# Optimization experiments

Hardware: AMD Instinct MI355X
Metric: run time of the kernel (lower is better)

The kernel has to match this reference:

```python
import jax, jax.numpy as jnp
import numpy as np

H, D = 8, 16
HD = H * D
SCALE0 = float(1.0 / np.sqrt(D * 1))   # degree-0 dot-product scale (order m=1)
SCALE1 = float(1.0 / np.sqrt(D * 3))   # degree-1 dot-product scale (order m=3)
SHARED = float(np.sqrt(0.5))           # shared_scale = sqrt(1/2) for DOT_PROD + SHARED
NEG = -1e9


def _split_heads_q(x):  # (b,n,HD,m) -> (b,H,n,D,m)
    b, n, _, m = x.shape
    return x.reshape(b, n, H, D, m).transpose(0, 2, 1, 3, 4)


def _split_heads_k(x):  # (b,n,N,HD,m) -> (b,H,n,N,D,m)
    b, n, N, _, m = x.shape
    return x.reshape(b, n, N, H, D, m).transpose(0, 3, 1, 2, 4, 5)


def _augment_kv(k, v, feats, W_self, null_k, null_v):
    # attend_self: VNLinear self key/value; use_null_kv: learned null tokens.
    b, n = feats.shape[:2]
    m = feats.shape[-1]
    skv = jnp.einsum('oc,bncm->bnom', W_self, feats)          # (b,n,2HD,m)
    sk, sv = jnp.split(skv, 2, axis=-2)
    sk = _split_heads_q(sk)[:, :, :, None]                     # (b,H,n,1,D,m)
    sv = _split_heads_q(sv)[:, :, :, None]
    nk = jnp.broadcast_to(null_k[None, :, None, None], (b, H, n, 1, D, m))
    nv = jnp.broadcast_to(null_v[None, :, None, None], (b, H, n, 1, D, m))
    k = jnp.concatenate([nk, sk, k], axis=3)                   # (b,H,n,2+N,D,m)
    v = jnp.concatenate([nv, sv, v], axis=3)
    return k, v


def _merge_heads(x):  # (b,H,n,D,m) -> (b,n,HD,m)
    b, _, n, _, m = x.shape
    return x.transpose(0, 2, 1, 3, 4).reshape(b, n, HD, m)


def _forward(q0, k0, v0, q1, k1, v1, feats0, feats1, edges,
             W_self_kv0, W_self_kv1, W_bias, self_bias, null_bias,
             null_k0, null_v0, null_k1, null_v1, head_weights1,
             W_out0, W_out1, neighbor_mask):
    b, n, N = edges.shape[:3]
    q0h, k0h, v0h = _split_heads_q(q0), _split_heads_k(k0), _split_heads_k(v0)
    q1h, k1h, v1h = _split_heads_q(q1), _split_heads_k(k1), _split_heads_k(v1)
    k0h, v0h = _augment_kv(k0h, v0h, feats0, W_self_kv0, null_k0, null_v0)
    k1h, v1h = _augment_kv(k1h, v1h, feats1, W_self_kv1, null_k1, null_v1)

    # pair bias for degree 0 (to_order==1); prepend null/self bias columns
    edge_bias = jnp.einsum('bnje,he->bhnj', edges, W_bias)     # (b,H,n,N)
    nb = jnp.broadcast_to(null_bias[None, :, None, None], (b, H, n, 1))
    sb = jnp.broadcast_to(self_bias[None, :, None, None], (b, H, n, 1))
    bias = jnp.concatenate([nb, sb, edge_bias], axis=-1)        # (b,H,n,2+N)

    sim0 = jnp.einsum('bhndm,bhnjdm->bhnj', q0h, k0h) * SCALE0 + bias
    w1 = jax.nn.softplus(head_weights1)                         # (1,H,1,1)
    sim1 = jnp.einsum('bhndm,bhnjdm->bhnj', q1h, k1h) * (SCALE1 * w1)

    total = (sim0 + sim1) * SHARED
    mask = jnp.concatenate(
        [jnp.ones((b, 1, n, 2), dtype=bool),                    # null + self always valid
         neighbor_mask[:, None]], axis=-1)
    total = jnp.where(mask, total, NEG)
    attn = jax.nn.softmax(total, axis=-1)                       # shared across degrees

    out0 = _merge_heads(jnp.einsum('bhnj,bhnjdm->bhndm', attn, v0h))
    out1 = _merge_heads(jnp.einsum('bhnj,bhnjdm->bhndm', attn, v1h))

    y0 = jnp.einsum('oc,bncm->bnom', W_out0, out0)              # FiberLinear deg 0
    y1 = jnp.einsum('oc,bncm->bnom', W_out1, out1)              # FiberLinear deg 1
    return y0, y1


def setup_inputs() -> dict:
    key = jax.random.key(0)
    ks = jax.random.split(key, 20)
    b, n, N, e = 1, 2048, 32, 32
    d0, d1 = 128, 64
    f = lambda k, s: jax.random.normal(k, s, dtype=jnp.float32) * 0.1
    return {
        'q0': f(ks[0], (b, n, HD, 1)), 'k0': f(ks[1], (b, n, N, HD, 1)), 'v0': f(ks[2], (b, n, N, HD, 1)),
        'q1': f(ks[3], (b, n, HD, 3)), 'k1': f(ks[4], (b, n, N, HD, 3)), 'v1': f(ks[5], (b, n, N, HD, 3)),
        'feats0': f(ks[6], (b, n, d0, 1)), 'feats1': f(ks[7], (b, n, d1, 3)),
        'edges': f(ks[8], (b, n, N, e)),
        'W_self_kv0': f(ks[9], (2 * HD, d0)), 'W_self_kv1': f(ks[10], (2 * HD, d1)),
        'W_bias': f(ks[11], (H, e)),
        'self_bias': jnp.zeros((H,), jnp.float32), 'null_bias': jnp.zeros((H,), jnp.float32),
        'null_k0': jnp.zeros((H, D, 1), jnp.float32), 'null_v0': jnp.zeros((H, D, 1), jnp.float32),
        'null_k1': jnp.zeros((H, D, 3), jnp.float32), 'null_v1': jnp.zeros((H, D, 3), jnp.float32),
        'head_weights1': jnp.full((1, H, 1, 1), float(np.log(np.e - 1.0)), jnp.float32),
        'W_out0': f(ks[12], (d0, HD)), 'W_out1': f(ks[13], (d1, HD)),
        'neighbor_mask': jax.random.uniform(ks[14], (b, n, N)) > 0.1,
    }


def reference(q0, k0, v0, q1, k1, v1, feats0, feats1, edges,
              W_self_kv0, W_self_kv1, W_bias, self_bias, null_bias,
              null_k0, null_v0, null_k1, null_v1, head_weights1,
              W_out0, W_out1, neighbor_mask):
    return _forward(q0, k0, v0, q1, k1, v1, feats0, feats1, edges,
                    W_self_kv0, W_self_kv1, W_bias, self_bias, null_bias,
                    null_k0, null_v0, null_k1, null_v1, head_weights1,
                    W_out0, W_out1, neighbor_mask)
```

## Files before the change

kernel.cpp:

```cpp
#include <hip/hip_runtime.h>
#include <hip/hip_bf16.h>

constexpr int kH  = 8;
constexpr int kD  = 16;
constexpr int kHD = 128;
constexpr int kN  = 32;
constexpr int kE  = 32;
constexpr int kD0 = 128;
constexpr int kD1 = 64;

constexpr float SCALE0   = 0.25f;
constexpr float SCALE1   = 0.14433756729740643f;
constexpr float SHARED_S = 0.70710678118654752f;
constexpr float NEGV     = -1e9f;


__global__ __launch_bounds__(256) void k1_selfkv(
    const float* __restrict__ q0, const float* __restrict__ q1,
    const float* __restrict__ feats0, const float* __restrict__ feats1,
    const float* __restrict__ Wskv0, const float* __restrict__ Wskv1,
    const float* __restrict__ self_bias, const float* __restrict__ null_bias,
    const float* __restrict__ nk0, const float* __restrict__ nk1,
    const float* __restrict__ hw1,
    float* __restrict__ ws_sc, float* __restrict__ ws_sv0, float* __restrict__ ws_sv1)
{
  const int i = blockIdx.x;
  const int t = threadIdx.x;
  __shared__ float f0s[kD0];
  __shared__ float f1s[kD1 * 3];
  __shared__ float q0s[kHD];
  __shared__ float q1s[kHD * 3];
  __shared__ float sk0[kHD];
  __shared__ float sk1[kHD * 3];
  __shared__ float w1s[kH];

  if (t < kD0)     f0s[t] = feats0[(size_t)i * kD0 + t];
  if (t < kD1 * 3) f1s[t] = feats1[(size_t)i * kD1 * 3 + t];
  if (t < kHD)     q0s[t] = q0[(size_t)i * kHD + t];
  for (int u = t; u < kHD * 3; u += 256) q1s[u] = q1[(size_t)i * kHD * 3 + u];
  if (t < kH) w1s[t] = log1pf(expf(hw1[t]));
  __syncthreads();

  float acc = 0.f;
  {
    const float4* wr = (const float4*)(Wskv0 + t * kD0);
    #pragma unroll
    for (int g = 0; g < 32; ++g) {
      float4 w = wr[g];
      int c = g * 4;
      acc += w.x * f0s[c] + w.y * f0s[c + 1] + w.z * f0s[c + 2] + w.w * f0s[c + 3];
    }
  }
  float a0 = 0.f, a1 = 0.f, a2 = 0.f;
  {
    const float4* wr = (const float4*)(Wskv1 + t * kD1);
    #pragma unroll
    for (int g = 0; g < 16; ++g) {
      float4 w = wr[g];
      int c = g * 4;
      a0 += w.x * f1s[(c + 0) * 3 + 0] + w.y * f1s[(c + 1) * 3 + 0]
          + w.z * f1s[(c + 2) * 3 + 0] + w.w * f1s[(c + 3) * 3 + 0];
      a1 += w.x * f1s[(c + 0) * 3 + 1] + w.y * f1s[(c + 1) * 3 + 1]
          + w.z * f1s[(c + 2) * 3 + 1] + w.w * f1s[(c + 3) * 3 + 1];
      a2 += w.x * f1s[(c + 0) * 3 + 2] + w.y * f1s[(c + 1) * 3 + 2]
          + w.z * f1s[(c + 2) * 3 + 2] + w.w * f1s[(c + 3) * 3 + 2];
    }
  }
  if (t < kHD) {
    sk0[t] = acc;
    sk1[t * 3 + 0] = a0; sk1[t * 3 + 1] = a1; sk1[t * 3 + 2] = a2;
  } else {
    const int o = t - kHD;
    ws_sv0[(size_t)i * kHD + o] = acc;
    float* sp = ws_sv1 + (size_t)i * kHD * 3 + o * 3;
    sp[0] = a0; sp[1] = a1; sp[2] = a2;
  }
  __syncthreads();

  if (t < 2 * kH) {
    const int h = t & 7;
    const bool is_self = t >= kH;
    float s0 = 0.f, s1 = 0.f, bias;
    if (is_self) {
      #pragma unroll
      for (int d = 0; d < kD; ++d) s0 += q0s[h * kD + d] * sk0[h * kD + d];
      #pragma unroll
      for (int x = 0; x < 48; ++x) s1 += q1s[h * 48 + x] * sk1[h * 48 + x];
      bias = self_bias[h];
    } else {
      #pragma unroll
      for (int d = 0; d < kD; ++d) s0 += q0s[h * kD + d] * nk0[h * kD + d];
      #pragma unroll
      for (int x = 0; x < 48; ++x) s1 += q1s[h * 48 + x] * nk1[h * 48 + x];
      bias = null_bias[h];
    }
    float total = (s0 * SCALE0 + bias + s1 * SCALE1 * w1s[h]) * SHARED_S;
    ws_sc[(size_t)i * 272 + h * 34 + (is_self ? 1 : 0)] = total;
  }
}

__global__ __launch_bounds__(256) void k2_sims(
    const float* __restrict__ q0, const float* __restrict__ q1,
    const float* __restrict__ k0, const float* __restrict__ k1,
    const float* __restrict__ edges, const float* __restrict__ Wbias,
    const float* __restrict__ hw1, const int* __restrict__ nmask,
    float* __restrict__ ws_sc)
{
  const int i = blockIdx.x;
  const int t = threadIdx.x;
  __shared__ float q0s[kH * 17];
  __shared__ float q1s[kH * 49];
  __shared__ float edg[kN * 33];
  __shared__ float wbT[kE * kH];
  __shared__ float w1s[kH];
  __shared__ float scL[kH][34];

  if (t < kHD) {
    int h = t >> 4, d = t & 15;
    q0s[h * 17 + d] = q0[(size_t)i * kHD + t];
  }
  for (int u = t; u < kHD * 3; u += 256) {
    int c = u / 3, m = u - c * 3;
    int h = c >> 4, d = c & 15;
    q1s[h * 49 + d * 3 + m] = q1[(size_t)i * kHD * 3 + u];
  }
  for (int u = t; u < kN * kE; u += 256) {
    int j = u >> 5, e = u & 31;
    edg[j * 33 + e] = edges[(size_t)i * kN * kE + u];
  }
  if (t < kH * kE) {
    int h = t >> 5, e = t & 31;
    wbT[e * 8 + h] = Wbias[t];
  }
  if (t < kH) w1s[t] = log1pf(expf(hw1[t]));
  if (t < 16) scL[t & 7][t >> 3] = ws_sc[(size_t)i * 272 + (t & 7) * 34 + (t >> 3)];
  __syncthreads();

  {
    const int j = t >> 3, h = t & 7;
    float bias = 0.f;
    #pragma unroll
    for (int e = 0; e < kE; ++e) bias += edg[j * 33 + e] * wbT[e * 8 + h];
    float s0 = 0.f;
    {
      const float4* kr = (const float4*)(k0 + (size_t)(i * kN + j) * kHD + h * kD);
      #pragma unroll
      for (int g = 0; g < 4; ++g) {
        float4 w = kr[g];
        int x = h * 17 + g * 4;
        s0 += w.x * q0s[x] + w.y * q0s[x + 1] + w.z * q0s[x + 2] + w.w * q0s[x + 3];
      }
    }
    float s1 = 0.f;
    {
      const float4* kr = (const float4*)(k1 + (size_t)(i * kN + j) * kHD * 3 + h * 48);
      #pragma unroll
      for (int g = 0; g < 12; ++g) {
        float4 w = kr[g];
        int x = h * 49 + g * 4;
        s1 += w.x * q1s[x] + w.y * q1s[x + 1] + w.z * q1s[x + 2] + w.w * q1s[x + 3];
      }
    }
    float total = (s0 * SCALE0 + bias + s1 * SCALE1 * w1s[h]) * SHARED_S;
    bool valid = nmask[(size_t)i * kN + j] != 0;
    scL[h][2 + j] = valid ? total : NEGV;
  }
  __syncthreads();

  if (t < kH) {
    float mx = -1e30f;
    #pragma unroll
    for (int j = 0; j < 34; ++j) mx = fmaxf(mx, scL[t][j]);
    float sum = 0.f;
    #pragma unroll
    for (int j = 0; j < 34; ++j) sum += __expf(scL[t][j] - mx);
    float inv = 1.f / sum;
    float* dst = ws_sc + (size_t)i * 272 + t * 34;
    #pragma unroll
    for (int j = 0; j < 34; ++j) dst[j] = __expf(scL[t][j] - mx) * inv;
  }
}

__global__ __launch_bounds__(256) void k3_out(
    const float* __restrict__ v0, const float* __restrict__ v1,
    const float* __restrict__ nv0, const float* __restrict__ nv1,
    const float* __restrict__ ws_sc,
    const float* __restrict__ ws_sv0, const float* __restrict__ ws_sv1,
    const float* __restrict__ Wout0, const float* __restrict__ Wout1,
    float* __restrict__ out, int n_total)
{
  const int i = blockIdx.x;
  const int t = threadIdx.x;
  __shared__ float o0[kHD];
  __shared__ float o1[kHD * 3];

  if (t < 64) {
    const int c0 = 2 * t;
    const int h = t >> 3;
    const float* at = ws_sc + (size_t)i * 272 + h * 34;
    float ax = at[0] * nv0[c0]     + at[1] * ws_sv0[(size_t)i * kHD + c0];
    float ay = at[0] * nv0[c0 + 1] + at[1] * ws_sv0[(size_t)i * kHD + c0 + 1];
    const float2* vp = (const float2*)(v0 + (size_t)i * kN * kHD) + t;
    #pragma unroll
    for (int j = 0; j < kN; ++j) {
      float2 p = vp[j * 64];
      float a = at[2 + j];
      ax += a * p.x; ay += a * p.y;
    }
    o0[c0] = ax; o0[c0 + 1] = ay;
  } else {
    const int u = t - 64;
    const int f0i = 2 * u;
    const int h = u / 24;
    const float* at = ws_sc + (size_t)i * 272 + h * 34;
    float ax = at[0] * nv1[f0i]     + at[1] * ws_sv1[(size_t)i * kHD * 3 + f0i];
    float ay = at[0] * nv1[f0i + 1] + at[1] * ws_sv1[(size_t)i * kHD * 3 + f0i + 1];
    const float2* vp = (const float2*)(v1 + (size_t)i * kN * kHD * 3) + u;
    #pragma unroll
    for (int j = 0; j < kN; ++j) {
      float2 p = vp[j * 192];
      float a = at[2 + j];
      ax += a * p.x; ay += a * p.y;
    }
    o1[f0i] = ax; o1[f0i + 1] = ay;
  }
  __syncthreads();

  for (int u = t; u < 320; u += 256) {
    if (u < 128) {
      float acc = 0.f;
      const float4* wr = (const float4*)(Wout0 + u * kHD);
      #pragma unroll
      for (int g = 0; g < 32; ++g) {
        float4 w = wr[g];
        int c = g * 4;
        acc += w.x * o0[c] + w.y * o0[c + 1] + w.z * o0[c + 2] + w.w * o0[c + 3];
      }
      out[(size_t)i * kHD + u] = acc;
    } else {
      const int v2 = u - 128;
      const int o = v2 / 3, m = v2 - o * 3;
      float acc = 0.f;
      const float4* wr = (const float4*)(Wout1 + o * kHD);
      #pragma unroll
      for (int g = 0; g < 32; ++g) {
        float4 w = wr[g];
        int c = g * 4;
        acc += w.x * o1[(c + 0) * 3 + m] + w.y * o1[(c + 1) * 3 + m]
             + w.z * o1[(c + 2) * 3 + m] + w.w * o1[(c + 3) * 3 + m];
      }
      out[(size_t)n_total * kHD + (size_t)i * 192 + v2] = acc;
    }
  }
}

extern "C" void kernel_launch(void* const* d_in, const int* in_sizes, int n_in,
                              void* d_out, int out_size, void* d_ws, size_t ws_size,
                              hipStream_t stream) {
  const int n = in_sizes[0] / kHD;
  const float* q0     = (const float*)d_in[0];
  const float* k0     = (const float*)d_in[1];
  const float* v0     = (const float*)d_in[2];
  const float* q1     = (const float*)d_in[3];
  const float* k1     = (const float*)d_in[4];
  const float* v1     = (const float*)d_in[5];
  const float* feats0 = (const float*)d_in[6];
  const float* feats1 = (const float*)d_in[7];
  const float* edges  = (const float*)d_in[8];
  const float* Wskv0  = (const float*)d_in[9];
  const float* Wskv1  = (const float*)d_in[10];
  const float* Wbias  = (const float*)d_in[11];
  const float* sbias  = (const float*)d_in[12];
  const float* nbias  = (const float*)d_in[13];
  const float* nk0    = (const float*)d_in[14];
  const float* nv0    = (const float*)d_in[15];
  const float* nk1    = (const float*)d_in[16];
  const float* nv1    = (const float*)d_in[17];
  const float* hw1    = (const float*)d_in[18];
  const float* Wout0  = (const float*)d_in[19];
  const float* Wout1  = (const float*)d_in[20];
  const int*   nmask  = (const int*)d_in[21];

  float* ws     = (float*)d_ws;
  float* ws_sc  = ws;
  float* ws_sv0 = ws + (size_t)n * 272;
  float* ws_sv1 = ws + (size_t)n * 272 + (size_t)n * 128;

  k1_selfkv<<<n, 256, 0, stream>>>(q0, q1, feats0, feats1, Wskv0, Wskv1,
                                   sbias, nbias, nk0, nk1, hw1,
                                   ws_sc, ws_sv0, ws_sv1);
  k2_sims<<<n, 256, 0, stream>>>(q0, q1, k0, k1, edges, Wbias, hw1, nmask, ws_sc);
  k3_out<<<n, 256, 0, stream>>>(v0, v1, nv0, nv1, ws_sc, ws_sv0, ws_sv1,
                                Wout0, Wout1, (float*)d_out, n);
}
```

Measured before the change: 389.6 us.

## Process four nodes per block to amortize weight loads across nodes

Each block in all three kernels now handles four nodes instead of one. The Wskv and Wout weight rows are loaded once and applied to four nodes' features, and global loads are widened to float4. k2 now stages the softmax result in shared memory and writes it out with vectorized stores. This cuts redundant weight traffic but quarters the grid size and increases register pressure. It also assumes n is divisible by 4.

```diff
diff --git a/kernel.cpp b/kernel.cpp
--- a/kernel.cpp
+++ b/kernel.cpp
@@ -1,5 +1,4 @@
 #include <hip/hip_runtime.h>
-#include <hip/hip_bf16.h>
 
 constexpr int kH  = 8;
 constexpr int kD  = 16;
@@ -8,6 +7,7 @@
 constexpr int kE  = 32;
 constexpr int kD0 = 128;
 constexpr int kD1 = 64;
+constexpr int kP  = 4;
 
 constexpr float SCALE0   = 0.25f;
 constexpr float SCALE1   = 0.14433756729740643f;
@@ -24,78 +24,97 @@
     const float* __restrict__ hw1,
     float* __restrict__ ws_sc, float* __restrict__ ws_sv0, float* __restrict__ ws_sv1)
 {
-  const int i = blockIdx.x;
-  const int t = threadIdx.x;
-  __shared__ float f0s[kD0];
-  __shared__ float f1s[kD1 * 3];
-  __shared__ float q0s[kHD];
-  __shared__ float q1s[kHD * 3];
-  __shared__ float sk0[kHD];
-  __shared__ float sk1[kHD * 3];
+  const int i0 = blockIdx.x * kP;
+  const int t  = threadIdx.x;
+  __shared__ __align__(16) float f0s[kP][kD0];
+  __shared__ __align__(16) float f1s[kP][kD1 * 3];
+  __shared__ __align__(16) float q0s[kP][kHD];
+  __shared__ __align__(16) float q1s[kP][kHD * 3];
+  __shared__ float sk0L[kP][kHD];
+  __shared__ float sk1L[kP][kHD * 3];
   __shared__ float w1s[kH];
 
-  if (t < kD0)     f0s[t] = feats0[(size_t)i * kD0 + t];
-  if (t < kD1 * 3) f1s[t] = feats1[(size_t)i * kD1 * 3 + t];
-  if (t < kHD)     q0s[t] = q0[(size_t)i * kHD + t];
-  for (int u = t; u < kHD * 3; u += 256) q1s[u] = q1[(size_t)i * kHD * 3 + u];
+  for (int u = t; u < kP * 32; u += 256) { int p = u >> 5, r = u & 31;
+    ((float4*)f0s[p])[r] = ((const float4*)(feats0 + (size_t)(i0 + p) * kD0))[r]; }
+  for (int u = t; u < kP * 48; u += 256) { int p = u / 48, r = u % 48;
+    ((float4*)f1s[p])[r] = ((const float4*)(feats1 + (size_t)(i0 + p) * kD1 * 3))[r]; }
+  for (int u = t; u < kP * 32; u += 256) { int p = u >> 5, r = u & 31;
+    ((float4*)q0s[p])[r] = ((const float4*)(q0 + (size_t)(i0 + p) * kHD))[r]; }
+  for (int u = t; u < kP * 96; u += 256) { int p = u / 96, r = u % 96;
+    ((float4*)q1s[p])[r] = ((const float4*)(q1 + (size_t)(i0 + p) * kHD * 3))[r]; }
   if (t < kH) w1s[t] = log1pf(expf(hw1[t]));
   __syncthreads();
 
-  float acc = 0.f;
+  float acc0[kP] = {};
   {
     const float4* wr = (const float4*)(Wskv0 + t * kD0);
     #pragma unroll
     for (int g = 0; g < 32; ++g) {
-      float4 w = wr[g];
-      int c = g * 4;
-      acc += w.x * f0s[c] + w.y * f0s[c + 1] + w.z * f0s[c + 2] + w.w * f0s[c + 3];
-    }
-  }
-  float a0 = 0.f, a1 = 0.f, a2 = 0.f;
+      float4 w = wr[g]; int c = g * 4;
+      #pragma unroll
+      for (int p = 0; p < kP; ++p)
+        acc0[p] += w.x * f0s[p][c] + w.y * f0s[p][c + 1]
+                 + w.z * f0s[p][c + 2] + w.w * f0s[p][c + 3];
+    }
+  }
+  float acc1[kP][3] = {};
   {
     const float4* wr = (const float4*)(Wskv1 + t * kD1);
     #pragma unroll
     for (int g = 0; g < 16; ++g) {
-      float4 w = wr[g];
-      int c = g * 4;
-      a0 += w.x * f1s[(c + 0) * 3 + 0] + w.y * f1s[(c + 1) * 3 + 0]
-          + w.z * f1s[(c + 2) * 3 + 0] + w.w * f1s[(c + 3) * 3 + 0];
-      a1 += w.x * f1s[(c + 0) * 3 + 1] + w.y * f1s[(c + 1) * 3 + 1]
-          + w.z * f1s[(c + 2) * 3 + 1] + w.w * f1s[(c + 3) * 3 + 1];
-      a2 += w.x * f1s[(c + 0) * 3 + 2] + w.y * f1s[(c + 1) * 3 + 2]
-          + w.z * f1s[(c + 2) * 3 + 2] + w.w * f1s[(c + 3) * 3 + 2];
+      float4 w = wr[g]; int c = g * 4;
+      float wv[4] = {w.x, w.y, w.z, w.w};
+      #pragma unroll
+      for (int q = 0; q < 4; ++q) {
+        #pragma unroll
+        for (int p = 0; p < kP; ++p) {
+          const float* fp = &f1s[p][(c + q) * 3];
+          acc1[p][0] += wv[q] * fp[0];
+          acc1[p][1] += wv[q] * fp[1];
+          acc1[p][2] += wv[q] * fp[2];
+        }
+      }
     }
   }
   if (t < kHD) {
-    sk0[t] = acc;
-    sk1[t * 3 + 0] = a0; sk1[t * 3 + 1] = a1; sk1[t * 3 + 2] = a2;
+    #pragma unroll
+    for (int p = 0; p < kP; ++p) {
+      sk0L[p][t] = acc0[p];
+      sk1L[p][t * 3 + 0] = acc1[p][0];
+      sk1L[p][t * 3 + 1] = acc1[p][1];
+      sk1L[p][t * 3 + 2] = acc1[p][2];
+    }
   } else {
     const int o = t - kHD;
-    ws_sv0[(size_t)i * kHD + o] = acc;
-    float* sp = ws_sv1 + (size_t)i * kHD * 3 + o * 3;
-    sp[0] = a0; sp[1] = a1; sp[2] = a2;
-  }
-  __syncthreads();
-
-  if (t < 2 * kH) {
-    const int h = t & 7;
-    const bool is_self = t >= kH;
+    #pragma unroll
+    for (int p = 0; p < kP; ++p) {
+      ws_sv0[(size_t)(i0 + p) * kHD + o] = acc0[p];
+      float* sp = ws_sv1 + (size_t)(i0 + p) * kHD * 3 + o * 3;
+      sp[0] = acc1[p][0]; sp[1] = acc1[p][1]; sp[2] = acc1[p][2];
+    }
+  }
+  __syncthreads();
+
+  if (t < kP * 16) {
+    const int p = t >> 4, idx = t & 15;
+    const int h = idx & 7;
+    const bool is_self = idx >= 8;
     float s0 = 0.f, s1 = 0.f, bias;
     if (is_self) {
       #pragma unroll
-      for (int d = 0; d < kD; ++d) s0 += q0s[h * kD + d] * sk0[h * kD + d];
-      #pragma unroll
-      for (int x = 0; x < 48; ++x) s1 += q1s[h * 48 + x] * sk1[h * 48 + x];
+      for (int d = 0; d < kD; ++d) s0 += q0s[p][h * kD + d] * sk0L[p][h * kD + d];
+      #pragma unroll
+      for (int x = 0; x < 48; ++x) s1 += q1s[p][h * 48 + x] * sk1L[p][h * 48 + x];
       bias = self_bias[h];
     } else {
       #pragma unroll
-      for (int d = 0; d < kD; ++d) s0 += q0s[h * kD + d] * nk0[h * kD + d];
-      #pragma unroll
-      for (int x = 0; x < 48; ++x) s1 += q1s[h * 48 + x] * nk1[h * 48 + x];
+      for (int d = 0; d < kD; ++d) s0 += q0s[p][h * kD + d] * nk0[h * kD + d];
+      #pragma unroll
+      for (int x = 0; x < 48; ++x) s1 += q1s[p][h * 48 + x] * nk1[h * 48 + x];
       bias = null_bias[h];
     }
     float total = (s0 * SCALE0 + bias + s1 * SCALE1 * w1s[h]) * SHARED_S;
-    ws_sc[(size_t)i * 272 + h * 34 + (is_self ? 1 : 0)] = total;
+    ws_sc[(size_t)(i0 + p) * 272 + h * 34 + (is_self ? 1 : 0)] = total;
   }
 }
 
@@ -106,78 +125,85 @@
     const float* __restrict__ hw1, const int* __restrict__ nmask,
     float* __restrict__ ws_sc)
 {
-  const int i = blockIdx.x;
-  const int t = threadIdx.x;
-  __shared__ float q0s[kH * 17];
-  __shared__ float q1s[kH * 49];
-  __shared__ float edg[kN * 33];
+  const int i0 = blockIdx.x * kP;
+  const int t  = threadIdx.x;
+  __shared__ float q0s[kP][kH * 17];
+  __shared__ float q1s[kP][kH * 49];
+  __shared__ float edg[kP][kN * 33];
   __shared__ float wbT[kE * kH];
   __shared__ float w1s[kH];
-  __shared__ float scL[kH][34];
-
-  if (t < kHD) {
-    int h = t >> 4, d = t & 15;
-    q0s[h * 17 + d] = q0[(size_t)i * kHD + t];
-  }
-  for (int u = t; u < kHD * 3; u += 256) {
-    int c = u / 3, m = u - c * 3;
-    int h = c >> 4, d = c & 15;
-    q1s[h * 49 + d * 3 + m] = q1[(size_t)i * kHD * 3 + u];
-  }
-  for (int u = t; u < kN * kE; u += 256) {
-    int j = u >> 5, e = u & 31;
-    edg[j * 33 + e] = edges[(size_t)i * kN * kE + u];
-  }
-  if (t < kH * kE) {
-    int h = t >> 5, e = t & 31;
-    wbT[e * 8 + h] = Wbias[t];
-  }
+  __shared__ __align__(16) float scL[kP][272];
+
+  for (int u = t; u < kP * 32; u += 256) { int p = u >> 5, r = u & 31;
+    float4 v = ((const float4*)(q0 + (size_t)(i0 + p) * kHD))[r];
+    int c = r * 4, h = c >> 4, d = c & 15;
+    float* dst = &q0s[p][h * 17 + d];
+    dst[0] = v.x; dst[1] = v.y; dst[2] = v.z; dst[3] = v.w; }
+  for (int u = t; u < kP * 96; u += 256) { int p = u / 96, r = u % 96;
+    float4 v = ((const float4*)(q1 + (size_t)(i0 + p) * kHD * 3))[r];
+    int c = r * 4, h = c / 48, x = c % 48;
+    float* dst = &q1s[p][h * 49 + x];
+    dst[0] = v.x; dst[1] = v.y; dst[2] = v.z; dst[3] = v.w; }
+  for (int u = t; u < kP * 256; u += 256) { int p = u >> 8, r = u & 255;
+    float4 v = ((const float4*)(edges + (size_t)(i0 + p) * kN * kE))[r];
+    int j = r >> 3, e4 = (r & 7) * 4;
+    float* dst = &edg[p][j * 33 + e4];
+    dst[0] = v.x; dst[1] = v.y; dst[2] = v.z; dst[3] = v.w; }
+  if (t < kH * kE) { int h = t >> 5, e = t & 31; wbT[e * 8 + h] = Wbias[t]; }
   if (t < kH) w1s[t] = log1pf(expf(hw1[t]));
-  if (t < 16) scL[t & 7][t >> 3] = ws_sc[(size_t)i * 272 + (t & 7) * 34 + (t >> 3)];
+  if (t < kP * 16) { int p = t >> 4, idx = t & 15, h = idx & 7, slot = idx >> 3;
+    scL[p][h * 34 + slot] = ws_sc[(size_t)(i0 + p) * 272 + h * 34 + slot]; }
   __syncthreads();
 
   {
     const int j = t >> 3, h = t & 7;
-    float bias = 0.f;
-    #pragma unroll
-    for (int e = 0; e < kE; ++e) bias += edg[j * 33 + e] * wbT[e * 8 + h];
-    float s0 = 0.f;
-    {
-      const float4* kr = (const float4*)(k0 + (size_t)(i * kN + j) * kHD + h * kD);
+    #pragma unroll
+    for (int p = 0; p < kP; ++p) {
+      const int i = i0 + p;
+      float bias = 0.f;
+      #pragma unroll
+      for (int e = 0; e < kE; ++e) bias += edg[p][j * 33 + e] * wbT[e * 8 + h];
+      float s0 = 0.f;
+      const float4* kr0 = (const float4*)(k0 + (size_t)(i * kN + j) * kHD + h * kD);
       #pragma unroll
       for (int g = 0; g < 4; ++g) {
-        float4 w = kr[g];
-        int x = h * 17 + g * 4;
-        s0 += w.x * q0s[x] + w.y * q0s[x + 1] + w.z * q0s[x + 2] + w.w * q0s[x + 3];
-      }
-    }
-    float s1 = 0.f;
-    {
-      const float4* kr = (const float4*)(k1 + (size_t)(i * kN + j) * kHD * 3 + h * 48);
+        float4 w = kr0[g]; int x = h * 17 + g * 4;
+        s0 += w.x * q0s[p][x] + w.y * q0s[p][x + 1]
+            + w.z * q0s[p][x + 2] + w.w * q0s[p][x + 3];
+      }
+      float s1 = 0.f;
+      const float4* kr1 = (const float4*)(k1 + (size_t)(i * kN + j) * kHD * 3 + h * 48);
       #pragma unroll
       for (int g = 0; g < 12; ++g) {
-        float4 w = kr[g];
-        int x = h * 49 + g * 4;
-        s1 += w.x * q1s[x] + w.y * q1s[x + 1] + w.z * q1s[x + 2] + w.w * q1s[x + 3];
-      }
-    }
-    float total = (s0 * SCALE0 + bias + s1 * SCALE1 * w1s[h]) * SHARED_S;
-    bool valid = nmask[(size_t)i * kN + j] != 0;
-    scL[h][2 + j] = valid ? total : NEGV;
-  }
-  __syncthreads();
-
-  if (t < kH) {
+        float4 w = kr1[g]; int x = h * 49 + g * 4;
+        s1 += w.x * q1s[p][x] + w.y * q1s[p][x + 1]
+            + w.z * q1s[p][x + 2] + w.w * q1s[p][x + 3];
+      }
+      float total = (s0 * SCALE0 + bias + s1 * SCALE1 * w1s[h]) * SHARED_S;
+      bool valid = nmask[(size_t)i * kN + j] != 0;
+      scL[p][h * 34 + 2 + j] = valid ? total : NEGV;
+    }
+  }
+  __syncthreads();
+
+  if (t < kP * kH) {
+    const int p = t >> 3, h = t & 7;
+    float* row = &scL[p][h * 34];
     float mx = -1e30f;
     #pragma unroll
-    for (int j = 0; j < 34; ++j) mx = fmaxf(mx, scL[t][j]);
+    for (int u = 0; u < 34; ++u) mx = fmaxf(mx, row[u]);
     float sum = 0.f;
     #pragma unroll
-    for (int j = 0; j < 34; ++j) sum += __expf(scL[t][j] - mx);
+    for (int u = 0; u < 34; ++u) sum += __expf(row[u] - mx);
     float inv = 1.f / sum;
-    float* dst = ws_sc + (size_t)i * 272 + t * 34;
-    #pragma unroll
-    for (int j = 0; j < 34; ++j) dst[j] = __expf(scL[t][j] - mx) * inv;
+    #pragma unroll
+    for (int u = 0; u < 34; ++u) row[u] = __expf(row[u] - mx) * inv;
+  }
+  __syncthreads();
+
+  for (int u = t; u < kP * 68; u += 256) {
+    int p = u / 68, r = u % 68;
+    ((float4*)(ws_sc + (size_t)(i0 + p) * 272))[r] = ((float4*)scL[p])[r];
   }
 }
 
@@ -189,67 +215,96 @@
     const float* __restrict__ Wout0, const float* __restrict__ Wout1,
     float* __restrict__ out, int n_total)
 {
-  const int i = blockIdx.x;
-  const int t = threadIdx.x;
-  __shared__ float o0[kHD];
-  __shared__ float o1[kHD * 3];
-
-  if (t < 64) {
-    const int c0 = 2 * t;
-    const int h = t >> 3;
-    const float* at = ws_sc + (size_t)i * 272 + h * 34;
-    float ax = at[0] * nv0[c0]     + at[1] * ws_sv0[(size_t)i * kHD + c0];
-    float ay = at[0] * nv0[c0 + 1] + at[1] * ws_sv0[(size_t)i * kHD + c0 + 1];
-    const float2* vp = (const float2*)(v0 + (size_t)i * kN * kHD) + t;
-    #pragma unroll
-    for (int j = 0; j < kN; ++j) {
-      float2 p = vp[j * 64];
-      float a = at[2 + j];
-      ax += a * p.x; ay += a * p.y;
-    }
-    o0[c0] = ax; o0[c0 + 1] = ay;
+  const int i0 = blockIdx.x * kP;
+  const int t  = threadIdx.x;
+  __shared__ __align__(16) float attnL[kP][272];
+  __shared__ __align__(16) float o0L[kP][kHD];
+  __shared__ __align__(16) float o1L[kP][kHD * 3];
+
+  for (int u = t; u < kP * 68; u += 256) {
+    int p = u / 68, r = u % 68;
+    ((float4*)attnL[p])[r] = ((const float4*)(ws_sc + (size_t)(i0 + p) * 272))[r];
+  }
+  __syncthreads();
+
+  const int half = t >> 7, slot = t & 127;
+  if (slot < 32) {
+    const int s = slot, h = s >> 2;
+    float4 nv = ((const float4*)nv0)[s];
+    #pragma unroll
+    for (int pi = 0; pi < 2; ++pi) {
+      const int p = half + pi * 2, i = i0 + p;
+      const float* at = attnL[p] + h * 34;
+      float4 sv = ((const float4*)(ws_sv0 + (size_t)i * kHD))[s];
+      float4 acc;
+      acc.x = at[0] * nv.x + at[1] * sv.x;
+      acc.y = at[0] * nv.y + at[1] * sv.y;
+      acc.z = at[0] * nv.z + at[1] * sv.z;
+      acc.w = at[0] * nv.w + at[1] * sv.w;
+      const float4* vp = (const float4*)(v0 + (size_t)i * kN * kHD) + s;
+      #pragma unroll
+      for (int j = 0; j < kN; ++j) {
+        float4 v = vp[j * 32];
+        float a = at[2 + j];
+        acc.x += a * v.x; acc.y += a * v.y; acc.z += a * v.z; acc.w += a * v.w;
+      }
+      ((float4*)o0L[p])[s] = acc;
+    }
   } else {
-    const int u = t - 64;
-    const int f0i = 2 * u;
-    const int h = u / 24;
-    const float* at = ws_sc + (size_t)i * 272 + h * 34;
-    float ax = at[0] * nv1[f0i]     + at[1] * ws_sv1[(size_t)i * kHD * 3 + f0i];
-    float ay = at[0] * nv1[f0i + 1] + at[1] * ws_sv1[(size_t)i * kHD * 3 + f0i + 1];
-    const float2* vp = (const float2*)(v1 + (size_t)i * kN * kHD * 3) + u;
-    #pragma unroll
-    for (int j = 0; j < kN; ++j) {
-      float2 p = vp[j * 192];
-      float a = at[2 + j];
-      ax += a * p.x; ay += a * p.y;
-    }
-    o1[f0i] = ax; o1[f0i + 1] = ay;
+    const int s = slot - 32;
+    const int h = s / 12;
+    float4 nv = ((const float4*)nv1)[s];
+    #pragma unroll
+    for (int pi = 0; pi < 2; ++pi) {
+      const int p = half + pi * 2, i = i0 + p;
+      const float* at = attnL[p] + h * 34;
+      float4 sv = ((const float4*)(ws_sv1 + (size_t)i * kHD * 3))[s];
+      float4 acc;
+      acc.x = at[0] * nv.x + at[1] * sv.x;
+      acc.y = at[0] * nv.y + at[1] * sv.y;
+      acc.z = at[0] * nv.z + at[1] * sv.z;
+      acc.w = at[0] * nv.w + at[1] * sv.w;
+      const float4* vp = (const float4*)(v1 + (size_t)i * kN * kHD * 3) + s;
+      #pragma unroll
+      for (int j = 0; j < kN; ++j) {
+        float4 v = vp[j * 96];
+        float a = at[2 + j];
+        acc.x += a * v.x; acc.y += a * v.y; acc.z += a * v.z; acc.w += a * v.w;
+      }
+      ((float4*)o1L[p])[s] = acc;
+    }
   }
   __syncthreads();
 
   for (int u = t; u < 320; u += 256) {
     if (u < 128) {
-      float acc = 0.f;
+      float acc[kP] = {};
       const float4* wr = (const float4*)(Wout0 + u * kHD);
       #pragma unroll
       for (int g = 0; g < 32; ++g) {
-        float4 w = wr[g];
-        int c = g * 4;
-        acc += w.x * o0[c] + w.y * o0[c + 1] + w.z * o0[c + 2] + w.w * o0[c + 3];
-      }
-      out[(size_t)i * kHD + u] = acc;
+        float4 w = wr[g]; int c = g * 4;
+        #pragma unroll
+        for (int p = 0; p < kP; ++p)
+          acc[p] += w.x * o0L[p][c] + w.y * o0L[p][c + 1]
+                  + w.z * o0L[p][c + 2] + w.w * o0L[p][c + 3];
+      }
+      #pragma unroll
+      for (int p = 0; p < kP; ++p) out[(size_t)(i0 + p) * kHD + u] = acc[p];
     } else {
-      const int v2 = u - 128;
-      const int o = v2 / 3, m = v2 - o * 3;
-      float acc = 0.f;
+      const int v2 = u - 128, o = v2 / 3, m = v2 - o * 3;
+      float acc[kP] = {};
       const float4* wr = (const float4*)(Wout1 + o * kHD);
       #pragma unroll
       for (int g = 0; g < 32; ++g) {
-        float4 w = wr[g];
-        int c = g * 4;
-        acc += w.x * o1[(c + 0) * 3 + m] + w.y * o1[(c + 1) * 3 + m]
-             + w.z * o1[(c + 2) * 3 + m] + w.w * o1[(c + 3) * 3 + m];
-      }
-      out[(size_t)n_total * kHD + (size_t)i * 192 + v2] = acc;
+        float4 w = wr[g]; int c = g * 4;
+        #pragma unroll
+        for (int p = 0; p < kP; ++p)
+          acc[p] += w.x * o1L[p][(c + 0) * 3 + m] + w.y * o1L[p][(c + 1) * 3 + m]
+                  + w.z * o1L[p][(c + 2) * 3 + m] + w.w * o1L[p][(c + 3) * 3 + m];
+      }
+      #pragma unroll
+      for (int p = 0; p < kP; ++p)
+        out[(size_t)n_total * kHD + (size_t)(i0 + p) * 192 + v2] = acc[p];
     }
   }
 }
@@ -258,6 +313,7 @@
                               void* d_out, int out_size, void* d_ws, size_t ws_size,
                               hipStream_t stream) {
   const int n = in_sizes[0] / kHD;
+  const int nb = n / kP;
   const float* q0     = (const float*)d_in[0];
   const float* k0     = (const float*)d_in[1];
   const float* v0     = (const float*)d_in[2];
@@ -286,10 +342,10 @@
   float* ws_sv0 = ws + (size_t)n * 272;
   float* ws_sv1 = ws + (size_t)n * 272 + (size_t)n * 128;
 
-  k1_selfkv<<<n, 256, 0, stream>>>(q0, q1, feats0, feats1, Wskv0, Wskv1,
-                                   sbias, nbias, nk0, nk1, hw1,
-                                   ws_sc, ws_sv0, ws_sv1);
-  k2_sims<<<n, 256, 0, stream>>>(q0, q1, k0, k1, edges, Wbias, hw1, nmask, ws_sc);
-  k3_out<<<n, 256, 0, stream>>>(v0, v1, nv0, nv1, ws_sc, ws_sv0, ws_sv1,
-                                Wout0, Wout1, (float*)d_out, n);
+  k1_selfkv<<<nb, 256, 0, stream>>>(q0, q1, feats0, feats1, Wskv0, Wskv1,
+                                    sbias, nbias, nk0, nk1, hw1,
+                                    ws_sc, ws_sv0, ws_sv1);
+  k2_sims<<<nb, 256, 0, stream>>>(q0, q1, k0, k1, edges, Wbias, hw1, nmask, ws_sc);
+  k3_out<<<nb, 256, 0, stream>>>(v0, v1, nv0, nv1, ws_sc, ws_sv0, ws_sv1,
+                                 Wout0, Wout1, (float*)d_out, n);
 }
```

New measurement: 382.0 us. About the same (-1.9%).
